# Kernel tuning notes

Measured on AMD Instinct MI355X. Metric: run time of the kernel, lower is better.

The kernel has to match this reference:

```python
import jax, jax.numpy as jnp
import numpy as np

N_NODES = 20000
N_EDGES = 80000
D = 128       # in_dim_node == in_dim_edge == hidden dims
ITERS = 15    # mp_iterations
EPS = 1e-5    # torch LayerNorm default eps


def _mlp(h, W0, b0, W1, b1, W2, b2, gamma, beta):
    """Linear-ReLU-Linear-ReLU-Linear-LayerNorm (hidden_layers=2)."""
    h = jax.nn.relu(h @ W0 + b0)
    h = jax.nn.relu(h @ W1 + b1)
    h = h @ W2 + b2
    mu = jnp.mean(h, axis=-1, keepdims=True)
    var = jnp.var(h, axis=-1, keepdims=True)
    return gamma * (h - mu) * jax.lax.rsqrt(var + EPS) + beta


def setup_inputs() -> dict:
    key = jax.random.key(0)
    ks = iter(jax.random.split(key, 32))

    def lin(fi, fo):
        bnd = 1.0 / np.sqrt(fi)
        W = jax.random.uniform(next(ks), (ITERS, fi, fo), minval=-bnd, maxval=bnd, dtype=jnp.float32)
        b = jax.random.uniform(next(ks), (ITERS, fo), minval=-bnd, maxval=bnd, dtype=jnp.float32)
        return W, b

    x = jax.random.normal(next(ks), (N_NODES, D), dtype=jnp.float32)
    edge_attr = jax.random.normal(next(ks), (N_EDGES, D), dtype=jnp.float32)
    edge_index = jax.random.randint(next(ks), (2, N_EDGES), 0, N_NODES)

    eW0, eB0 = lin(3 * D, D)   # edge MLP input = cat(src, dest, edge) = 384
    eW1, eB1 = lin(D, D)
    eW2, eB2 = lin(D, D)
    nW0, nB0 = lin(2 * D, D)   # node MLP input = cat(x, agg) = 256
    nW1, nB1 = lin(D, D)
    nW2, nB2 = lin(D, D)
    ones = jnp.ones((ITERS, D), jnp.float32)
    zeros = jnp.zeros((ITERS, D), jnp.float32)

    return dict(x=x, edge_attr=edge_attr,
                eW0=eW0, eB0=eB0, eW1=eW1, eB1=eB1, eW2=eW2, eB2=eB2, eG=ones, eBeta=zeros,
                nW0=nW0, nB0=nB0, nW1=nW1, nB1=nB1, nW2=nW2, nB2=nB2, nG=ones, nBeta=zeros,
                edge_index=edge_index)


def reference(x, edge_attr, eW0, eB0, eW1, eB1, eW2, eB2, eG, eBeta,
              nW0, nB0, nW1, nB1, nW2, nB2, nG, nBeta, edge_index):
    row, col = edge_index[0], edge_index[1]
    n = x.shape[0]
    params = (eW0, eB0, eW1, eB1, eW2, eB2, eG, eBeta,
              nW0, nB0, nW1, nB1, nW2, nB2, nG, nBeta)

    def step(carry, p):
        xc, ec = carry
        (ew0, eb0, ew1, eb1, ew2, eb2, eg, ebt,
         nw0, nb0, nw1, nb1, nw2, nb2, ng, nbt) = p
        # EdgeProcessor: gather + MLP, then FullResidualConnection (add previous)
        e_in = jnp.concatenate([xc[row], xc[col], ec], axis=-1)        # [E, 3D]
        ec = _mlp(e_in, ew0, eb0, ew1, eb1, ew2, eb2, eg, ebt) + ec
        # NodeProcessor: scatter_sum over destination nodes + MLP + residual
        agg = jax.ops.segment_sum(ec, col, num_segments=n)             # [N, D]
        n_in = jnp.concatenate([xc, agg], axis=-1)                     # [N, 2D]
        xc = _mlp(n_in, nw0, nb0, nw1, nb1, nw2, nb2, ng, nbt) + xc
        return (xc, ec), None

    (x, edge_attr), _ = jax.lax.scan(step, (x, edge_attr), params)
    return x, edge_attr
```

## Files before the change

### kernel.cpp

```cpp
#include <hip/hip_runtime.h>
#include <hip/hip_bf16.h>

typedef __hip_bfloat16 bf16;
typedef __attribute__((ext_vector_type(8))) short short8;
typedef __attribute__((ext_vector_type(4))) float f32x4;

#define NN 20000
#define NE 80000
#define DD 128
#define NITER 15
#define HSTRIDE 136

__device__ inline void gload16(const void* g, void* l) {
  __builtin_amdgcn_global_load_lds(
      (const __attribute__((address_space(1))) void*)g,
      (__attribute__((address_space(3))) void*)l, 16, 0, 0);
}

__device__ inline float bfbits2f(unsigned int hi16) {
  union { unsigned int u; float f; } c; c.u = hi16; return c.f;
}

__global__ void detect_kernel(const unsigned short* __restrict__ p, int nhalf,
                              int* __restrict__ flag) {
  __shared__ int cs[256], ct[256];
  const int t = threadIdx.x;
  int sane = 0, tot = 0;
  for (int i = 2 * t; i < nhalf; i += 512) {
    unsigned short v = p[i];
    int e = (v >> 7) & 0xFF;
    tot++;
    if (v == 0 || (e >= 80 && e <= 170)) sane++;
  }
  cs[t] = sane; ct[t] = tot;
  __syncthreads();
  for (int o = 128; o > 0; o >>= 1) {
    if (t < o) { cs[t] += cs[t + o]; ct[t] += ct[t + o]; }
    __syncthreads();
  }
  if (t == 0) *flag = (cs[0] * 10 > ct[0] * 7) ? 1 : 0;
}

__global__ void in2fb_kernel(const void* __restrict__ src, float* __restrict__ dstf,
                             bf16* __restrict__ dstb, int n, const int* __restrict__ flag) {
  int i = blockIdx.x * 256 + threadIdx.x;
  if (i < n) {
    float v = (*flag) ? (float)((const bf16*)src)[i] : ((const float*)src)[i];
    dstf[i] = v;
    dstb[i] = (bf16)v;
  }
}

__global__ void in2f_kernel(const void* __restrict__ src, float* __restrict__ dst,
                            int n, const int* __restrict__ flag) {
  int i = blockIdx.x * 256 + threadIdx.x;
  if (i < n) {
    dst[i] = (*flag) ? (float)((const bf16*)src)[i] : ((const float*)src)[i];
  }
}

__global__ void w2t_kernel(const void* __restrict__ W, bf16* __restrict__ Wt,
                           int K, const int* __restrict__ flag) {
  int i = blockIdx.x * 256 + threadIdx.x;
  int total = NITER * K * DD;
  if (i < total) {
    float v = (*flag) ? (float)((const bf16*)W)[i] : ((const float*)W)[i];
    int t = i / (K * DD);
    int rem = i - t * K * DD;
    int k = rem >> 7;
    int n = rem & 127;
    Wt[(size_t)t * K * DD + (size_t)n * K + k] = (bf16)v;
  }
}

__global__ void outw_kernel(const float* __restrict__ xf, const float* __restrict__ ef,
                            void* __restrict__ out, const int* __restrict__ flag) {
  int i = blockIdx.x * 256 + threadIdx.x;
  const int nx = NN * DD, total = (NN + NE) * DD;
  if (i < total) {
    float v = (i < nx) ? xf[i] : ef[i - nx];
    if (*flag) ((bf16*)out)[i] = (bf16)v;
    else       ((float*)out)[i] = v;
  }
}

template<int K0, int AMODE>
__global__ __launch_bounds__(256, 3) void fused_mlp(
    const bf16*  __restrict__ S0b,
    const bf16*  __restrict__ S1b,
    const int*   __restrict__ eidx,
    const bf16*  __restrict__ W0t,
    const bf16*  __restrict__ W1t,
    const bf16*  __restrict__ W2t,
    const float* __restrict__ b0,
    const float* __restrict__ b1,
    const float* __restrict__ b2,
    const float* __restrict__ gamma,
    const float* __restrict__ beta,
    float*       __restrict__ stf,
    bf16*        __restrict__ stb,
    int M)
{
  __shared__ __align__(16) bf16 Bls[2][128 * 32];
  __shared__ __align__(16) bf16 Hls[128 * HSTRIDE];

  const int tid  = threadIdx.x;
  const int lane = tid & 63;
  const int wv   = tid >> 6;
  const int l15  = lane & 15, quad = lane >> 4;
  const int m0   = blockIdx.x * 128;

  const int scol = tid >> 2;
  const int sk8  = (tid & 3) * 8;

  int rowm[2], ir[2], ic[2];
#pragma unroll
  for (int mi = 0; mi < 2; mi++) {
    rowm[mi] = min(m0 + wv * 32 + mi * 16 + l15, M - 1);
    if (AMODE == 1) { ir[mi] = eidx[rowm[mi]]; ic[mi] = eidx[NE + rowm[mi]]; }
  }

  auto dmaW = [&](const bf16* W, int K, int kk, int buf) {
    gload16(W + (size_t)scol * K + kk + sk8,        &Bls[buf][scol * 32 + sk8]);
    gload16(W + (size_t)(scol + 64) * K + kk + sk8, &Bls[buf][(scol + 64) * 32 + sk8]);
  };
  auto gatherA = [&](int kk, short8 a[2]) {
    const int ks = (kk & 127) + quad * 8;
#pragma unroll
    for (int mi = 0; mi < 2; mi++) {
      const bf16* base;
      if (AMODE == 1) {
        const int seg = kk >> 7;
        base = (seg == 0) ? S0b + (size_t)ir[mi] * DD
             : (seg == 1) ? S0b + (size_t)ic[mi] * DD
                          : S1b + (size_t)rowm[mi] * DD;
      } else {
        base = (kk >> 7) ? S1b + (size_t)rowm[mi] * DD
                         : S0b + (size_t)rowm[mi] * DD;
      }
      a[mi] = *(const short8*)(base + ks);
    }
  };

  f32x4 acc[2][8];
  auto zacc = [&]() {
#pragma unroll
    for (int i = 0; i < 2; i++)
#pragma unroll
      for (int j = 0; j < 8; j++) acc[i][j] = (f32x4){0.f, 0.f, 0.f, 0.f};
  };
  auto slabMfmaA = [&](const short8 a[2], int buf) {
    short8 bfr[8];
#pragma unroll
    for (int ni = 0; ni < 8; ni++)
      bfr[ni] = *(const short8*)&Bls[buf][(ni * 16 + l15) * 32 + quad * 8];
#pragma unroll
    for (int mi = 0; mi < 2; mi++)
#pragma unroll
      for (int ni = 0; ni < 8; ni++)
        acc[mi][ni] = __builtin_amdgcn_mfma_f32_16x16x32_bf16(a[mi], bfr[ni], acc[mi][ni], 0, 0, 0);
  };
  auto slabMfmaH = [&](int kk, int buf) {
    short8 a[2], bfr[8];
#pragma unroll
    for (int mi = 0; mi < 2; mi++)
      a[mi] = *(const short8*)&Hls[(wv * 32 + mi * 16 + l15) * HSTRIDE + kk + quad * 8];
#pragma unroll
    for (int ni = 0; ni < 8; ni++)
      bfr[ni] = *(const short8*)&Bls[buf][(ni * 16 + l15) * 32 + quad * 8];
#pragma unroll
    for (int mi = 0; mi < 2; mi++)
#pragma unroll
      for (int ni = 0; ni < 8; ni++)
        acc[mi][ni] = __builtin_amdgcn_mfma_f32_16x16x32_bf16(a[mi], bfr[ni], acc[mi][ni], 0, 0, 0);
  };
  auto writeH = [&](const float* bias) {
    float bv[8];
#pragma unroll
    for (int ni = 0; ni < 8; ni++) bv[ni] = bias[ni * 16 + l15];
#pragma unroll
    for (int mi = 0; mi < 2; mi++)
#pragma unroll
      for (int r = 0; r < 4; r++) {
        const int row = wv * 32 + mi * 16 + quad * 4 + r;
#pragma unroll
        for (int ni = 0; ni < 8; ni++)
          Hls[row * HSTRIDE + ni * 16 + l15] = (bf16)fmaxf(acc[mi][ni][r] + bv[ni], 0.f);
      }
  };

  constexpr int NS1 = K0 / 32;

  zacc();
  short8 aCur[2], aNxt[2];
  dmaW(W0t, K0, 0, 0);
  gatherA(0, aCur);
  __syncthreads();
#pragma unroll
  for (int s = 0; s < NS1; s++) {
    if (s + 1 < NS1) {
      dmaW(W0t, K0, (s + 1) * 32, (s + 1) & 1);
      gatherA((s + 1) * 32, aNxt);
    } else {
      dmaW(W1t, 128, 0, NS1 & 1);
    }
    slabMfmaA(aCur, s & 1);
    __syncthreads();
    aCur[0] = aNxt[0]; aCur[1] = aNxt[1];
  }
  writeH(b0);
  __syncthreads();

  zacc();
#pragma unroll
  for (int s = 0; s < 4; s++) {
    if (s < 3) dmaW(W1t, 128, (s + 1) * 32, (NS1 + s + 1) & 1);
    else       dmaW(W2t, 128, 0,            (NS1 + 4) & 1);
    slabMfmaH(s * 32, (NS1 + s) & 1);
    __syncthreads();
  }
  writeH(b1);
  __syncthreads();

  zacc();
#pragma unroll
  for (int s = 0; s < 4; s++) {
    if (s < 3) dmaW(W2t, 128, (s + 1) * 32, (NS1 + 4 + s + 1) & 1);
    slabMfmaH(s * 32, (NS1 + 4 + s) & 1);
    if (s < 3) __syncthreads();
  }

  float bv[8], gv[8], btv[8];
#pragma unroll
  for (int ni = 0; ni < 8; ni++) {
    const int col = ni * 16 + l15;
    bv[ni] = b2[col]; gv[ni] = gamma[col]; btv[ni] = beta[col];
  }
#pragma unroll
  for (int mi = 0; mi < 2; mi++)
#pragma unroll
    for (int r = 0; r < 4; r++) {
      float a = 0.f, bq = 0.f;
#pragma unroll
      for (int ni = 0; ni < 8; ni++) {
        const float v = acc[mi][ni][r] + bv[ni];
        a += v; bq += v * v;
      }
#pragma unroll
      for (int off = 1; off < 16; off <<= 1) {
        a  += __shfl_xor(a, off);
        bq += __shfl_xor(bq, off);
      }
      const float mu = a * (1.0f / 128.0f);
      const float var = fmaxf(bq * (1.0f / 128.0f) - mu * mu, 0.0f);
      const float rs = rsqrtf(var + 1e-5f);
      const int m = m0 + wv * 32 + mi * 16 + quad * 4 + r;
      if (m < M) {
#pragma unroll
        for (int ni = 0; ni < 8; ni++) {
          const int col = ni * 16 + l15;
          const float v = acc[mi][ni][r] + bv[ni];
          const float lnv = (v - mu) * rs * gv[ni] + btv[ni];
          const size_t idx = (size_t)m * DD + col;
          const float nv = lnv + stf[idx];
          stf[idx] = nv;
          stb[idx] = (bf16)nv;
        }
      }
    }
}

__global__ void zero_kernel(int* __restrict__ p, int n) {
  int i = blockIdx.x * 256 + threadIdx.x;
  if (i < n) p[i] = 0;
}

__global__ void hist_kernel(const int* __restrict__ eidx, int* __restrict__ counts) {
  int e = blockIdx.x * 256 + threadIdx.x;
  if (e < NE) atomicAdd(&counts[eidx[NE + e]], 1);
}

__global__ void scan_kernel(const int* __restrict__ counts, int* __restrict__ offs,
                            int* __restrict__ cursor) {
  __shared__ int sums[1024];
  const int t = threadIdx.x;
  const int base = t * 20;
  int local[20];
  int s = 0;
  for (int i = 0; i < 20; i++) {
    int idx = base + i;
    int c = (idx < NN) ? counts[idx] : 0;
    local[i] = s; s += c;
  }
  sums[t] = s;
  __syncthreads();
  for (int off = 1; off < 1024; off <<= 1) {
    int v = 0;
    if (t >= off) v = sums[t - off];
    __syncthreads();
    if (t >= off) sums[t] += v;
    __syncthreads();
  }
  int excl = (t == 0) ? 0 : sums[t - 1];
  for (int i = 0; i < 20; i++) {
    int idx = base + i;
    if (idx < NN) { offs[idx] = excl + local[i]; cursor[idx] = 0; }
  }
  if (t == 1023) offs[NN] = sums[1023];
}

__global__ void fill_kernel(const int* __restrict__ eidx, const int* __restrict__ offs,
                            int* __restrict__ cursor, int* __restrict__ sorted) {
  int e = blockIdx.x * 256 + threadIdx.x;
  if (e < NE) {
    int n = eidx[NE + e];
    int p = atomicAdd(&cursor[n], 1);
    sorted[offs[n] + p] = e;
  }
}

__global__ void aggregate_kernel(const bf16* __restrict__ eb, const int* __restrict__ offs,
                                 const int* __restrict__ sorted, bf16* __restrict__ aggb) {
  const int node = blockIdx.x * 4 + (threadIdx.x >> 6);
  const int lane = threadIdx.x & 63;
  if (node >= NN) return;
  const int s = offs[node], t = offs[node + 1];
  float a0 = 0.f, a1 = 0.f;
  for (int i = s; i < t; i++) {
    const int e = sorted[i];
    unsigned int v = *(const unsigned int*)(eb + (size_t)e * DD + 2 * lane);
    a0 += bfbits2f(v << 16);
    a1 += bfbits2f(v & 0xFFFF0000u);
  }
  bf16 o0 = (bf16)a0, o1 = (bf16)a1;
  unsigned int pack = (unsigned int)(*(unsigned short*)&o0)
                    | ((unsigned int)(*(unsigned short*)&o1) << 16);
  *(unsigned int*)(aggb + (size_t)node * DD + 2 * lane) = pack;
}

extern "C" void kernel_launch(void* const* d_in, const int* in_sizes, int n_in,
                              void* d_out, int out_size, void* d_ws, size_t ws_size,
                              hipStream_t stream) {
  const void* x_in = d_in[0];
  const void* e_in = d_in[1];
  const void* eW0 = d_in[2];
  const void* eB0 = d_in[3];
  const void* eW1 = d_in[4];
  const void* eB1 = d_in[5];
  const void* eW2 = d_in[6];
  const void* eB2 = d_in[7];
  const void* eG  = d_in[8];
  const void* eBt = d_in[9];
  const void* nW0 = d_in[10];
  const void* nB0 = d_in[11];
  const void* nW1 = d_in[12];
  const void* nB1 = d_in[13];
  const void* nW2 = d_in[14];
  const void* nB2 = d_in[15];
  const void* nG  = d_in[16];
  const void* nBt = d_in[17];
  const int*  eidx = (const int*)d_in[18];

  char* ws = (char*)d_ws;
  size_t off = 0;
  auto alloc = [&](size_t bytes) -> char* {
    char* p = ws + off;
    off = (off + bytes + 255) & ~(size_t)255;
    return p;
  };

  float* xf   = (float*)alloc((size_t)NN * DD * 4);
  float* ef   = (float*)alloc((size_t)NE * DD * 4);
  bf16*  xb   = (bf16*)alloc((size_t)NN * DD * 2);
  bf16*  eb   = (bf16*)alloc((size_t)NE * DD * 2);
  bf16*  aggb = (bf16*)alloc((size_t)NN * DD * 2);
  bf16*  eW0t = (bf16*)alloc((size_t)NITER * 384 * DD * 2);
  bf16*  eW1t = (bf16*)alloc((size_t)NITER * 128 * DD * 2);
  bf16*  eW2t = (bf16*)alloc((size_t)NITER * 128 * DD * 2);
  bf16*  nW0t = (bf16*)alloc((size_t)NITER * 256 * DD * 2);
  bf16*  nW1t = (bf16*)alloc((size_t)NITER * 128 * DD * 2);
  bf16*  nW2t = (bf16*)alloc((size_t)NITER * 128 * DD * 2);
  const int NB = NITER * DD;
  float* eB0f = (float*)alloc(NB * 4);
  float* eB1f = (float*)alloc(NB * 4);
  float* eB2f = (float*)alloc(NB * 4);
  float* eGf  = (float*)alloc(NB * 4);
  float* eBtf = (float*)alloc(NB * 4);
  float* nB0f = (float*)alloc(NB * 4);
  float* nB1f = (float*)alloc(NB * 4);
  float* nB2f = (float*)alloc(NB * 4);
  float* nGf  = (float*)alloc(NB * 4);
  float* nBtf = (float*)alloc(NB * 4);
  int* counts = (int*)alloc((size_t)NN * 4);
  int* cursor = (int*)alloc((size_t)NN * 4);
  int* offs   = (int*)alloc((size_t)(NN + 1) * 4);
  int* sorted = (int*)alloc((size_t)NE * 4);
  int* flag   = (int*)alloc(4);

  detect_kernel<<<1, 256, 0, stream>>>((const unsigned short*)x_in, 16384, flag);

  in2fb_kernel<<<(NN * DD + 255) / 256, 256, 0, stream>>>(x_in, xf, xb, NN * DD, flag);
  in2fb_kernel<<<(NE * DD + 255) / 256, 256, 0, stream>>>(e_in, ef, eb, NE * DD, flag);
  w2t_kernel<<<(NITER * 384 * DD + 255) / 256, 256, 0, stream>>>(eW0, eW0t, 384, flag);
  w2t_kernel<<<(NITER * 128 * DD + 255) / 256, 256, 0, stream>>>(eW1, eW1t, 128, flag);
  w2t_kernel<<<(NITER * 128 * DD + 255) / 256, 256, 0, stream>>>(eW2, eW2t, 128, flag);
  w2t_kernel<<<(NITER * 256 * DD + 255) / 256, 256, 0, stream>>>(nW0, nW0t, 256, flag);
  w2t_kernel<<<(NITER * 128 * DD + 255) / 256, 256, 0, stream>>>(nW1, nW1t, 128, flag);
  w2t_kernel<<<(NITER * 128 * DD + 255) / 256, 256, 0, stream>>>(nW2, nW2t, 128, flag);
  in2f_kernel<<<(NB + 255) / 256, 256, 0, stream>>>(eB0, eB0f, NB, flag);
  in2f_kernel<<<(NB + 255) / 256, 256, 0, stream>>>(eB1, eB1f, NB, flag);
  in2f_kernel<<<(NB + 255) / 256, 256, 0, stream>>>(eB2, eB2f, NB, flag);
  in2f_kernel<<<(NB + 255) / 256, 256, 0, stream>>>(eG,  eGf,  NB, flag);
  in2f_kernel<<<(NB + 255) / 256, 256, 0, stream>>>(eBt, eBtf, NB, flag);
  in2f_kernel<<<(NB + 255) / 256, 256, 0, stream>>>(nB0, nB0f, NB, flag);
  in2f_kernel<<<(NB + 255) / 256, 256, 0, stream>>>(nB1, nB1f, NB, flag);
  in2f_kernel<<<(NB + 255) / 256, 256, 0, stream>>>(nB2, nB2f, NB, flag);
  in2f_kernel<<<(NB + 255) / 256, 256, 0, stream>>>(nG,  nGf,  NB, flag);
  in2f_kernel<<<(NB + 255) / 256, 256, 0, stream>>>(nBt, nBtf, NB, flag);

  zero_kernel<<<(NN + 255) / 256, 256, 0, stream>>>(counts, NN);
  hist_kernel<<<(NE + 255) / 256, 256, 0, stream>>>(eidx, counts);
  scan_kernel<<<1, 1024, 0, stream>>>(counts, offs, cursor);
  fill_kernel<<<(NE + 255) / 256, 256, 0, stream>>>(eidx, offs, cursor, sorted);

  const int egrid = NE / 128;
  const int ngrid = (NN + 127) / 128;

  for (int t = 0; t < NITER; t++) {
    fused_mlp<384, 1><<<egrid, 256, 0, stream>>>(
        xb, eb, eidx,
        eW0t + (size_t)t * 384 * DD, eW1t + (size_t)t * 128 * DD, eW2t + (size_t)t * 128 * DD,
        eB0f + t * DD, eB1f + t * DD, eB2f + t * DD,
        eGf + t * DD, eBtf + t * DD, ef, eb, NE);
    aggregate_kernel<<<(NN + 3) / 4, 256, 0, stream>>>(eb, offs, sorted, aggb);
    fused_mlp<256, 2><<<ngrid, 256, 0, stream>>>(
        xb, aggb, nullptr,
        nW0t + (size_t)t * 256 * DD, nW1t + (size_t)t * 128 * DD, nW2t + (size_t)t * 128 * DD,
        nB0f + t * DD, nB1f + t * DD, nB2f + t * DD,
        nGf + t * DD, nBtf + t * DD, xf, xb, NN);
  }

  outw_kernel<<<((NN + NE) * DD + 255) / 256, 256, 0, stream>>>(xf, ef, d_out, flag);
}
```

Before: 1.295 ms.

## Keep residual state in bf16 only and shrink node MLP tile to 64 rows

Removes the fp32 shadow copies of node and edge features, so the fused MLP epilogue reads and writes the residual only in bf16, and the output kernel converts from bf16. This cuts global memory traffic in the edge and node kernels. The node MLP is templated on tile height and launched with 64-row tiles to fill more CUs. The cost is that the residual accumulates in bf16 rounding over 15 iterations, which may raise the error.

```diff
diff --git a/kernel.cpp b/kernel.cpp
--- a/kernel.cpp
+++ b/kernel.cpp
@@ -41,13 +41,12 @@
   if (t == 0) *flag = (cs[0] * 10 > ct[0] * 7) ? 1 : 0;
 }
 
-__global__ void in2fb_kernel(const void* __restrict__ src, float* __restrict__ dstf,
-                             bf16* __restrict__ dstb, int n, const int* __restrict__ flag) {
+__global__ void in2b_kernel(const void* __restrict__ src, bf16* __restrict__ dst,
+                            int n, const int* __restrict__ flag) {
   int i = blockIdx.x * 256 + threadIdx.x;
   if (i < n) {
     float v = (*flag) ? (float)((const bf16*)src)[i] : ((const float*)src)[i];
-    dstf[i] = v;
-    dstb[i] = (bf16)v;
+    dst[i] = (bf16)v;
   }
 }
 
@@ -73,18 +72,18 @@
   }
 }
 
-__global__ void outw_kernel(const float* __restrict__ xf, const float* __restrict__ ef,
-                            void* __restrict__ out, const int* __restrict__ flag) {
+__global__ void outwb_kernel(const bf16* __restrict__ xb, const bf16* __restrict__ eb,
+                             void* __restrict__ out, const int* __restrict__ flag) {
   int i = blockIdx.x * 256 + threadIdx.x;
   const int nx = NN * DD, total = (NN + NE) * DD;
   if (i < total) {
-    float v = (i < nx) ? xf[i] : ef[i - nx];
-    if (*flag) ((bf16*)out)[i] = (bf16)v;
-    else       ((float*)out)[i] = v;
-  }
-}
-
-template<int K0, int AMODE>
+    bf16 v = (i < nx) ? xb[i] : eb[i - nx];
+    if (*flag) ((bf16*)out)[i] = v;
+    else       ((float*)out)[i] = (float)v;
+  }
+}
+
+template<int K0, int AMODE, int TM>
 __global__ __launch_bounds__(256, 3) void fused_mlp(
     const bf16*  __restrict__ S0b,
     const bf16*  __restrict__ S1b,
@@ -97,26 +96,28 @@
     const float* __restrict__ b2,
     const float* __restrict__ gamma,
     const float* __restrict__ beta,
-    float*       __restrict__ stf,
-    bf16*        __restrict__ stb,
+    bf16*        __restrict__ st,
     int M)
 {
+  constexpr int MI = TM / 64;
+  constexpr int WB = TM / 4;
+
   __shared__ __align__(16) bf16 Bls[2][128 * 32];
-  __shared__ __align__(16) bf16 Hls[128 * HSTRIDE];
+  __shared__ __align__(16) bf16 Hls[TM * HSTRIDE];
 
   const int tid  = threadIdx.x;
   const int lane = tid & 63;
   const int wv   = tid >> 6;
   const int l15  = lane & 15, quad = lane >> 4;
-  const int m0   = blockIdx.x * 128;
+  const int m0   = blockIdx.x * TM;
 
   const int scol = tid >> 2;
   const int sk8  = (tid & 3) * 8;
 
-  int rowm[2], ir[2], ic[2];
-#pragma unroll
-  for (int mi = 0; mi < 2; mi++) {
-    rowm[mi] = min(m0 + wv * 32 + mi * 16 + l15, M - 1);
+  int rowm[MI], ir[MI], ic[MI];
+#pragma unroll
+  for (int mi = 0; mi < MI; mi++) {
+    rowm[mi] = min(m0 + wv * WB + mi * 16 + l15, M - 1);
     if (AMODE == 1) { ir[mi] = eidx[rowm[mi]]; ic[mi] = eidx[NE + rowm[mi]]; }
   }
 
@@ -124,10 +125,10 @@
     gload16(W + (size_t)scol * K + kk + sk8,        &Bls[buf][scol * 32 + sk8]);
     gload16(W + (size_t)(scol + 64) * K + kk + sk8, &Bls[buf][(scol + 64) * 32 + sk8]);
   };
-  auto gatherA = [&](int kk, short8 a[2]) {
+  auto gatherA = [&](int kk, short8 a[MI]) {
     const int ks = (kk & 127) + quad * 8;
 #pragma unroll
-    for (int mi = 0; mi < 2; mi++) {
+    for (int mi = 0; mi < MI; mi++) {
       const bf16* base;
       if (AMODE == 1) {
         const int seg = kk >> 7;
@@ -142,34 +143,34 @@
     }
   };
 
-  f32x4 acc[2][8];
+  f32x4 acc[MI][8];
   auto zacc = [&]() {
 #pragma unroll
-    for (int i = 0; i < 2; i++)
+    for (int i = 0; i < MI; i++)
 #pragma unroll
       for (int j = 0; j < 8; j++) acc[i][j] = (f32x4){0.f, 0.f, 0.f, 0.f};
   };
-  auto slabMfmaA = [&](const short8 a[2], int buf) {
+  auto slabMfmaA = [&](const short8 a[MI], int buf) {
     short8 bfr[8];
 #pragma unroll
     for (int ni = 0; ni < 8; ni++)
       bfr[ni] = *(const short8*)&Bls[buf][(ni * 16 + l15) * 32 + quad * 8];
 #pragma unroll
-    for (int mi = 0; mi < 2; mi++)
+    for (int mi = 0; mi < MI; mi++)
 #pragma unroll
       for (int ni = 0; ni < 8; ni++)
         acc[mi][ni] = __builtin_amdgcn_mfma_f32_16x16x32_bf16(a[mi], bfr[ni], acc[mi][ni], 0, 0, 0);
   };
   auto slabMfmaH = [&](int kk, int buf) {
-    short8 a[2], bfr[8];
-#pragma unroll
-    for (int mi = 0; mi < 2; mi++)
-      a[mi] = *(const short8*)&Hls[(wv * 32 + mi * 16 + l15) * HSTRIDE + kk + quad * 8];
+    short8 a[MI], bfr[8];
+#pragma unroll
+    for (int mi = 0; mi < MI; mi++)
+      a[mi] = *(const short8*)&Hls[(wv * WB + mi * 16 + l15) * HSTRIDE + kk + quad * 8];
 #pragma unroll
     for (int ni = 0; ni < 8; ni++)
       bfr[ni] = *(const short8*)&Bls[buf][(ni * 16 + l15) * 32 + quad * 8];
 #pragma unroll
-    for (int mi = 0; mi < 2; mi++)
+    for (int mi = 0; mi < MI; mi++)
 #pragma unroll
       for (int ni = 0; ni < 8; ni++)
         acc[mi][ni] = __builtin_amdgcn_mfma_f32_16x16x32_bf16(a[mi], bfr[ni], acc[mi][ni], 0, 0, 0);
@@ -179,10 +180,10 @@
 #pragma unroll
     for (int ni = 0; ni < 8; ni++) bv[ni] = bias[ni * 16 + l15];
 #pragma unroll
-    for (int mi = 0; mi < 2; mi++)
+    for (int mi = 0; mi < MI; mi++)
 #pragma unroll
       for (int r = 0; r < 4; r++) {
-        const int row = wv * 32 + mi * 16 + quad * 4 + r;
+        const int row = wv * WB + mi * 16 + quad * 4 + r;
 #pragma unroll
         for (int ni = 0; ni < 8; ni++)
           Hls[row * HSTRIDE + ni * 16 + l15] = (bf16)fmaxf(acc[mi][ni][r] + bv[ni], 0.f);
@@ -192,7 +193,7 @@
   constexpr int NS1 = K0 / 32;
 
   zacc();
-  short8 aCur[2], aNxt[2];
+  short8 aCur[MI], aNxt[MI];
   dmaW(W0t, K0, 0, 0);
   gatherA(0, aCur);
   __syncthreads();
@@ -206,7 +207,8 @@
     }
     slabMfmaA(aCur, s & 1);
     __syncthreads();
-    aCur[0] = aNxt[0]; aCur[1] = aNxt[1];
+#pragma unroll
+    for (int mi = 0; mi < MI; mi++) aCur[mi] = aNxt[mi];
   }
   writeH(b0);
   __syncthreads();
@@ -237,7 +239,7 @@
     bv[ni] = b2[col]; gv[ni] = gamma[col]; btv[ni] = beta[col];
   }
 #pragma unroll
-  for (int mi = 0; mi < 2; mi++)
+  for (int mi = 0; mi < MI; mi++)
 #pragma unroll
     for (int r = 0; r < 4; r++) {
       float a = 0.f, bq = 0.f;
@@ -254,7 +256,7 @@
       const float mu = a * (1.0f / 128.0f);
       const float var = fmaxf(bq * (1.0f / 128.0f) - mu * mu, 0.0f);
       const float rs = rsqrtf(var + 1e-5f);
-      const int m = m0 + wv * 32 + mi * 16 + quad * 4 + r;
+      const int m = m0 + wv * WB + mi * 16 + quad * 4 + r;
       if (m < M) {
 #pragma unroll
         for (int ni = 0; ni < 8; ni++) {
@@ -262,9 +264,7 @@
           const float v = acc[mi][ni][r] + bv[ni];
           const float lnv = (v - mu) * rs * gv[ni] + btv[ni];
           const size_t idx = (size_t)m * DD + col;
-          const float nv = lnv + stf[idx];
-          stf[idx] = nv;
-          stb[idx] = (bf16)nv;
+          st[idx] = (bf16)(lnv + (float)st[idx]);
         }
       }
     }
@@ -369,8 +369,6 @@
     return p;
   };
 
-  float* xf   = (float*)alloc((size_t)NN * DD * 4);
-  float* ef   = (float*)alloc((size_t)NE * DD * 4);
   bf16*  xb   = (bf16*)alloc((size_t)NN * DD * 2);
   bf16*  eb   = (bf16*)alloc((size_t)NE * DD * 2);
   bf16*  aggb = (bf16*)alloc((size_t)NN * DD * 2);
@@ -399,8 +397,8 @@
 
   detect_kernel<<<1, 256, 0, stream>>>((const unsigned short*)x_in, 16384, flag);
 
-  in2fb_kernel<<<(NN * DD + 255) / 256, 256, 0, stream>>>(x_in, xf, xb, NN * DD, flag);
-  in2fb_kernel<<<(NE * DD + 255) / 256, 256, 0, stream>>>(e_in, ef, eb, NE * DD, flag);
+  in2b_kernel<<<(NN * DD + 255) / 256, 256, 0, stream>>>(x_in, xb, NN * DD, flag);
+  in2b_kernel<<<(NE * DD + 255) / 256, 256, 0, stream>>>(e_in, eb, NE * DD, flag);
   w2t_kernel<<<(NITER * 384 * DD + 255) / 256, 256, 0, stream>>>(eW0, eW0t, 384, flag);
   w2t_kernel<<<(NITER * 128 * DD + 255) / 256, 256, 0, stream>>>(eW1, eW1t, 128, flag);
   w2t_kernel<<<(NITER * 128 * DD + 255) / 256, 256, 0, stream>>>(eW2, eW2t, 128, flag);
@@ -424,21 +422,21 @@
   fill_kernel<<<(NE + 255) / 256, 256, 0, stream>>>(eidx, offs, cursor, sorted);
 
   const int egrid = NE / 128;
-  const int ngrid = (NN + 127) / 128;
+  const int ngrid = (NN + 63) / 64;
 
   for (int t = 0; t < NITER; t++) {
-    fused_mlp<384, 1><<<egrid, 256, 0, stream>>>(
+    fused_mlp<384, 1, 128><<<egrid, 256, 0, stream>>>(
         xb, eb, eidx,
         eW0t + (size_t)t * 384 * DD, eW1t + (size_t)t * 128 * DD, eW2t + (size_t)t * 128 * DD,
         eB0f + t * DD, eB1f + t * DD, eB2f + t * DD,
-        eGf + t * DD, eBtf + t * DD, ef, eb, NE);
+        eGf + t * DD, eBtf + t * DD, eb, NE);
     aggregate_kernel<<<(NN + 3) / 4, 256, 0, stream>>>(eb, offs, sorted, aggb);
-    fused_mlp<256, 2><<<ngrid, 256, 0, stream>>>(
+    fused_mlp<256, 2, 64><<<ngrid, 256, 0, stream>>>(
         xb, aggb, nullptr,
         nW0t + (size_t)t * 256 * DD, nW1t + (size_t)t * 128 * DD, nW2t + (size_t)t * 128 * DD,
         nB0f + t * DD, nB1f + t * DD, nB2f + t * DD,
-        nGf + t * DD, nBtf + t * DD, xf, xb, NN);
-  }
-
-  outw_kernel<<<((NN + NE) * DD + 255) / 256, 256, 0, stream>>>(xf, ef, d_out, flag);
-}
+        nGf + t * DD, nBtf + t * DD, xb, NN);
+  }
+
+  outwb_kernel<<<((NN + NE) * DD + 255) / 256, 256, 0, stream>>>(xb, eb, d_out, flag);
+}
```

After: 1.145 ms. -11.6%, faster.
